# Performance work log

Hardware: AMD Instinct MI355X
Metric: run time of the kernel (lower is better)

## Reference

```python
import jax, jax.numpy as jnp
import numpy as np

# tf.image.rgb_to_grayscale luminance weights
_RGB_W = jnp.array([0.2989, 0.5870, 0.1140], dtype=jnp.float32)
# LBP weight kernel (row-major over the 3x3 neighborhood)
_LBP_K = jnp.array([[1.0, 2.0, 4.0],
                    [128.0, 0.0, 8.0],
                    [64.0, 32.0, 16.0]], dtype=jnp.float32)


def setup_inputs() -> dict:
    key = jax.random.key(0)
    inputs = jax.random.uniform(key, (32, 512, 512, 3), dtype=jnp.float32)
    return {"inputs": inputs}


def reference(inputs):
    # inputs: [N, H, W, 3]
    gray = jnp.tensordot(inputs, _RGB_W, axes=[[-1], [0]])  # [N, H, W]
    N, H, W = gray.shape
    padded = jnp.pad(gray, ((0, 0), (1, 1), (1, 1)))  # SAME zero padding
    # extract_patches(3x3, SAME) -> 9 channels in row-major (dy, dx) order
    patches = jnp.stack(
        [padded[:, dy:dy + H, dx:dx + W] for dy in range(3) for dx in range(3)],
        axis=-1,
    )  # [N, H, W, 9]
    center = patches[..., 4:5]
    binary = jnp.where(patches >= center, 1.0, 0.0)  # [N, H, W, 9]
    # Original conv2d tiles the SAME 3x3 spatial kernel across all 9 input
    # channels, so it equals: (sum over channels) then a 3x3 weighted sum.
    s = binary.sum(axis=-1)  # [N, H, W]
    sp = jnp.pad(s, ((0, 0), (1, 1), (1, 1)))  # SAME zero padding for conv
    lbp = sum(
        _LBP_K[dy, dx] * sp[:, dy:dy + H, dx:dx + W]
        for dy in range(3) for dx in range(3)
        if _LBP_K[dy, dx] != 0.0
    )
    return lbp[..., None]  # [N, H, W, 1]
```

## Files before the change

kernel.cpp:

```cpp
#include <hip/hip_runtime.h>


#define TPB    256
#define TILE_X 64
#define TILE_Y 32
#define GROWS  36
#define GCOLS  72
#define SROWS  34
#define SCOLS  68

typedef float f32x4 __attribute__((ext_vector_type(4)));

__global__ __launch_bounds__(TPB) void lbp_kernel(const float* __restrict__ in,
                                                  float* __restrict__ out) {
    __shared__ float grayS[GROWS * GCOLS];
    __shared__ float sS[SROWS * SCOLS];

    const int n   = blockIdx.z;
    const int y0  = blockIdx.y * TILE_Y;
    const int x0  = blockIdx.x * TILE_X;
    const int tid = threadIdx.x;

    #pragma unroll
    for (int k = 0; k < 3; ++k) {
        const int i = tid + k * TPB;
        if (i < GROWS * (GCOLS / 4)) {
            const int qy  = i / (GCOLS / 4);
            const int qx  = i - qy * (GCOLS / 4);
            const int gy  = y0 - 2 + qy;
            const int px0 = x0 - 4 + qx * 4;
            const bool oky = (unsigned)gy  < 512u;
            const bool okx = (unsigned)px0 < 512u;
            const int  cy  = min(max(gy, 0), 511);
            const int  cx  = okx ? px0 : 0;
            const f32x4* p4 = reinterpret_cast<const f32x4*>(
                in + ((size_t)(n * 512 + cy) * 512 + (size_t)cx) * 3);
            const f32x4 f0 = p4[0];
            const f32x4 f1 = p4[1];
            const f32x4 f2 = p4[2];
            const bool ok = okx & oky;
            const float g0 = __builtin_fmaf(f0.z, 0.114f, __builtin_fmaf(f0.y, 0.587f, f0.x * 0.2989f));
            const float g1 = __builtin_fmaf(f1.y, 0.114f, __builtin_fmaf(f1.x, 0.587f, f0.w * 0.2989f));
            const float g2 = __builtin_fmaf(f2.x, 0.114f, __builtin_fmaf(f1.w, 0.587f, f1.z * 0.2989f));
            const float g3 = __builtin_fmaf(f2.w, 0.114f, __builtin_fmaf(f2.z, 0.587f, f2.y * 0.2989f));
            f32x4 gv;
            gv.x = ok ? g0 : 0.0f;
            gv.y = ok ? g1 : 0.0f;
            gv.z = ok ? g2 : 0.0f;
            gv.w = ok ? g3 : 0.0f;
            *reinterpret_cast<f32x4*>(&grayS[qy * GCOLS + qx * 4]) = gv;
        }
    }
    __syncthreads();

    #pragma unroll
    for (int k = 0; k < 3; ++k) {
        const int i = tid + k * TPB;
        if (i < SROWS * (SCOLS / 4)) {
            const int ly  = i / (SCOLS / 4);
            const int lx0 = (i - ly * (SCOLS / 4)) * 4;
            const f32x4 a0 = *reinterpret_cast<const f32x4*>(&grayS[(ly + 0) * GCOLS + lx0]);
            const f32x4 b0 = *reinterpret_cast<const f32x4*>(&grayS[(ly + 0) * GCOLS + lx0 + 4]);
            const f32x4 a1 = *reinterpret_cast<const f32x4*>(&grayS[(ly + 1) * GCOLS + lx0]);
            const f32x4 b1 = *reinterpret_cast<const f32x4*>(&grayS[(ly + 1) * GCOLS + lx0 + 4]);
            const f32x4 a2 = *reinterpret_cast<const f32x4*>(&grayS[(ly + 2) * GCOLS + lx0]);
            const f32x4 b2 = *reinterpret_cast<const f32x4*>(&grayS[(ly + 2) * GCOLS + lx0 + 4]);
            const float r0[8] = {a0.x, a0.y, a0.z, a0.w, b0.x, b0.y, b0.z, b0.w};
            const float r1[8] = {a1.x, a1.y, a1.z, a1.w, b1.x, b1.y, b1.z, b1.w};
            const float r2[8] = {a2.x, a2.y, a2.z, a2.w, b2.x, b2.y, b2.z, b2.w};
            float sv[4];
            #pragma unroll
            for (int e = 0; e < 4; ++e) {
                const float c = r1[3 + e];
                float s = 0.0f;
                #pragma unroll
                for (int d = 0; d < 3; ++d) {
                    s += (r0[2 + e + d] >= c) ? 1.0f : 0.0f;
                    s += (r1[2 + e + d] >= c) ? 1.0f : 0.0f;
                    s += (r2[2 + e + d] >= c) ? 1.0f : 0.0f;
                }
                const bool ok = ((unsigned)(y0 - 1 + ly) < 512u) &
                                ((unsigned)(x0 - 1 + lx0 + e) < 512u);
                sv[e] = ok ? s : 0.0f;
            }
            f32x4 svv;
            svv.x = sv[0]; svv.y = sv[1]; svv.z = sv[2]; svv.w = sv[3];
            *reinterpret_cast<f32x4*>(&sS[ly * SCOLS + lx0]) = svv;
        }
    }
    __syncthreads();

    #pragma unroll
    for (int k = 0; k < 2; ++k) {
        const int i   = tid + k * TPB;
        const int py  = i / (TILE_X / 4);
        const int px0 = (i - py * (TILE_X / 4)) * 4;
        const f32x4 a0 = *reinterpret_cast<const f32x4*>(&sS[(py + 0) * SCOLS + px0]);
        const f32x4 b0 = *reinterpret_cast<const f32x4*>(&sS[(py + 0) * SCOLS + px0 + 4]);
        const f32x4 a1 = *reinterpret_cast<const f32x4*>(&sS[(py + 1) * SCOLS + px0]);
        const f32x4 b1 = *reinterpret_cast<const f32x4*>(&sS[(py + 1) * SCOLS + px0 + 4]);
        const f32x4 a2 = *reinterpret_cast<const f32x4*>(&sS[(py + 2) * SCOLS + px0]);
        const f32x4 b2 = *reinterpret_cast<const f32x4*>(&sS[(py + 2) * SCOLS + px0 + 4]);
        const float r0[8] = {a0.x, a0.y, a0.z, a0.w, b0.x, b0.y, b0.z, b0.w};
        const float r1[8] = {a1.x, a1.y, a1.z, a1.w, b1.x, b1.y, b1.z, b1.w};
        const float r2[8] = {a2.x, a2.y, a2.z, a2.w, b2.x, b2.y, b2.z, b2.w};
        f32x4 ov;
        #pragma unroll
        for (int e = 0; e < 4; ++e) {
            ov[e] =   1.0f * r0[e] +   2.0f * r0[e + 1] +  4.0f * r0[e + 2]
                  + 128.0f * r1[e] +                        8.0f * r1[e + 2]
                  +  64.0f * r2[e] +  32.0f * r2[e + 1] + 16.0f * r2[e + 2];
        }
        f32x4* dst = reinterpret_cast<f32x4*>(
            out + (size_t)(n * 512 + (y0 + py)) * 512 + (size_t)(x0 + px0));
        __builtin_nontemporal_store(ov, dst);
    }
}

extern "C" void kernel_launch(void* const* d_in, const int* in_sizes, int n_in,
                              void* d_out, int out_size, void* d_ws, size_t ws_size,
                              hipStream_t stream) {
    const float* in = (const float*)d_in[0];
    float* out = (float*)d_out;
    dim3 grid(512 / TILE_X, 512 / TILE_Y, 32);
    dim3 block(TPB);
    lbp_kernel<<<grid, block, 0, stream>>>(in, out);
}
```

Before: 31.33 us.

## Process two images per block and prefetch the second image's input during compute

```diff
diff --git a/kernel.cpp b/kernel.cpp
--- a/kernel.cpp
+++ b/kernel.cpp
@@ -8,113 +8,152 @@
 #define GCOLS  72
 #define SROWS  34
 #define SCOLS  68
+#define GQ     (GROWS * (GCOLS / 4))
+#define SQ     (SROWS * (SCOLS / 4))
 
 typedef float f32x4 __attribute__((ext_vector_type(4)));
 
-__global__ __launch_bounds__(TPB) void lbp_kernel(const float* __restrict__ in,
-                                                  float* __restrict__ out) {
+__global__ __launch_bounds__(TPB, 5) void lbp_kernel(const float* __restrict__ in,
+                                                     float* __restrict__ out) {
     __shared__ float grayS[GROWS * GCOLS];
     __shared__ float sS[SROWS * SCOLS];
 
-    const int n   = blockIdx.z;
     const int y0  = blockIdx.y * TILE_Y;
     const int x0  = blockIdx.x * TILE_X;
     const int tid = threadIdx.x;
+    const int n0  = blockIdx.z;
+    const int n1  = blockIdx.z + 16;
 
-    #pragma unroll
-    for (int k = 0; k < 3; ++k) {
-        const int i = tid + k * TPB;
-        if (i < GROWS * (GCOLS / 4)) {
-            const int qy  = i / (GCOLS / 4);
-            const int qx  = i - qy * (GCOLS / 4);
-            const int gy  = y0 - 2 + qy;
-            const int px0 = x0 - 4 + qx * 4;
-            const bool oky = (unsigned)gy  < 512u;
-            const bool okx = (unsigned)px0 < 512u;
-            const int  cy  = min(max(gy, 0), 511);
-            const int  cx  = okx ? px0 : 0;
-            const f32x4* p4 = reinterpret_cast<const f32x4*>(
-                in + ((size_t)(n * 512 + cy) * 512 + (size_t)cx) * 3);
-            const f32x4 f0 = p4[0];
-            const f32x4 f1 = p4[1];
-            const f32x4 f2 = p4[2];
-            const bool ok = okx & oky;
-            const float g0 = __builtin_fmaf(f0.z, 0.114f, __builtin_fmaf(f0.y, 0.587f, f0.x * 0.2989f));
-            const float g1 = __builtin_fmaf(f1.y, 0.114f, __builtin_fmaf(f1.x, 0.587f, f0.w * 0.2989f));
-            const float g2 = __builtin_fmaf(f2.x, 0.114f, __builtin_fmaf(f1.w, 0.587f, f1.z * 0.2989f));
-            const float g3 = __builtin_fmaf(f2.w, 0.114f, __builtin_fmaf(f2.z, 0.587f, f2.y * 0.2989f));
-            f32x4 gv;
-            gv.x = ok ? g0 : 0.0f;
-            gv.y = ok ? g1 : 0.0f;
-            gv.z = ok ? g2 : 0.0f;
-            gv.w = ok ? g3 : 0.0f;
-            *reinterpret_cast<f32x4*>(&grayS[qy * GCOLS + qx * 4]) = gv;
+    f32x4 L[3][3];
+
+    auto issue = [&](int n) {
+        #pragma unroll
+        for (int k = 0; k < 3; ++k) {
+            const int i = tid + k * TPB;
+            if (i < GQ) {
+                const int qy  = i / (GCOLS / 4);
+                const int qx  = i - qy * (GCOLS / 4);
+                const int gy  = y0 - 2 + qy;
+                const int px0 = x0 - 4 + qx * 4;
+                const bool okx = (unsigned)px0 < 512u;
+                const int  cy  = min(max(gy, 0), 511);
+                const int  cx  = okx ? px0 : 0;
+                const f32x4* p4 = reinterpret_cast<const f32x4*>(
+                    in + ((size_t)(n * 512 + cy) * 512 + (size_t)cx) * 3);
+                L[k][0] = p4[0];
+                L[k][1] = p4[1];
+                L[k][2] = p4[2];
+            }
         }
-    }
-    __syncthreads();
+    };
 
-    #pragma unroll
-    for (int k = 0; k < 3; ++k) {
-        const int i = tid + k * TPB;
-        if (i < SROWS * (SCOLS / 4)) {
-            const int ly  = i / (SCOLS / 4);
-            const int lx0 = (i - ly * (SCOLS / 4)) * 4;
-            const f32x4 a0 = *reinterpret_cast<const f32x4*>(&grayS[(ly + 0) * GCOLS + lx0]);
-            const f32x4 b0 = *reinterpret_cast<const f32x4*>(&grayS[(ly + 0) * GCOLS + lx0 + 4]);
-            const f32x4 a1 = *reinterpret_cast<const f32x4*>(&grayS[(ly + 1) * GCOLS + lx0]);
-            const f32x4 b1 = *reinterpret_cast<const f32x4*>(&grayS[(ly + 1) * GCOLS + lx0 + 4]);
-            const f32x4 a2 = *reinterpret_cast<const f32x4*>(&grayS[(ly + 2) * GCOLS + lx0]);
-            const f32x4 b2 = *reinterpret_cast<const f32x4*>(&grayS[(ly + 2) * GCOLS + lx0 + 4]);
+    auto store_gray = [&]() {
+        #pragma unroll
+        for (int k = 0; k < 3; ++k) {
+            const int i = tid + k * TPB;
+            if (i < GQ) {
+                const int qy  = i / (GCOLS / 4);
+                const int qx  = i - qy * (GCOLS / 4);
+                const int gy  = y0 - 2 + qy;
+                const int px0 = x0 - 4 + qx * 4;
+                const bool ok = ((unsigned)gy < 512u) & ((unsigned)px0 < 512u);
+                const f32x4 f0 = L[k][0], f1 = L[k][1], f2 = L[k][2];
+                const float g0 = __builtin_fmaf(f0.z, 0.114f, __builtin_fmaf(f0.y, 0.587f, f0.x * 0.2989f));
+                const float g1 = __builtin_fmaf(f1.y, 0.114f, __builtin_fmaf(f1.x, 0.587f, f0.w * 0.2989f));
+                const float g2 = __builtin_fmaf(f2.x, 0.114f, __builtin_fmaf(f1.w, 0.587f, f1.z * 0.2989f));
+                const float g3 = __builtin_fmaf(f2.w, 0.114f, __builtin_fmaf(f2.z, 0.587f, f2.y * 0.2989f));
+                f32x4 gv;
+                gv.x = ok ? g0 : 0.0f;
+                gv.y = ok ? g1 : 0.0f;
+                gv.z = ok ? g2 : 0.0f;
+                gv.w = ok ? g3 : 0.0f;
+                *reinterpret_cast<f32x4*>(&grayS[qy * GCOLS + qx * 4]) = gv;
+            }
+        }
+    };
+
+    auto compute_s = [&]() {
+        #pragma unroll
+        for (int k = 0; k < 3; ++k) {
+            const int i = tid + k * TPB;
+            if (i < SQ) {
+                const int ly  = i / (SCOLS / 4);
+                const int lx0 = (i - ly * (SCOLS / 4)) * 4;
+                const f32x4 a0 = *reinterpret_cast<const f32x4*>(&grayS[(ly + 0) * GCOLS + lx0]);
+                const f32x4 b0 = *reinterpret_cast<const f32x4*>(&grayS[(ly + 0) * GCOLS + lx0 + 4]);
+                const f32x4 a1 = *reinterpret_cast<const f32x4*>(&grayS[(ly + 1) * GCOLS + lx0]);
+                const f32x4 b1 = *reinterpret_cast<const f32x4*>(&grayS[(ly + 1) * GCOLS + lx0 + 4]);
+                const f32x4 a2 = *reinterpret_cast<const f32x4*>(&grayS[(ly + 2) * GCOLS + lx0]);
+                const f32x4 b2 = *reinterpret_cast<const f32x4*>(&grayS[(ly + 2) * GCOLS + lx0 + 4]);
+                const float r0[8] = {a0.x, a0.y, a0.z, a0.w, b0.x, b0.y, b0.z, b0.w};
+                const float r1[8] = {a1.x, a1.y, a1.z, a1.w, b1.x, b1.y, b1.z, b1.w};
+                const float r2[8] = {a2.x, a2.y, a2.z, a2.w, b2.x, b2.y, b2.z, b2.w};
+                float sv[4];
+                #pragma unroll
+                for (int e = 0; e < 4; ++e) {
+                    const float c = r1[3 + e];
+                    float s = 0.0f;
+                    #pragma unroll
+                    for (int d = 0; d < 3; ++d) {
+                        s += (r0[2 + e + d] >= c) ? 1.0f : 0.0f;
+                        s += (r1[2 + e + d] >= c) ? 1.0f : 0.0f;
+                        s += (r2[2 + e + d] >= c) ? 1.0f : 0.0f;
+                    }
+                    const bool ok = ((unsigned)(y0 - 1 + ly) < 512u) &
+                                    ((unsigned)(x0 - 1 + lx0 + e) < 512u);
+                    sv[e] = ok ? s : 0.0f;
+                }
+                f32x4 svv;
+                svv.x = sv[0]; svv.y = sv[1]; svv.z = sv[2]; svv.w = sv[3];
+                *reinterpret_cast<f32x4*>(&sS[ly * SCOLS + lx0]) = svv;
+            }
+        }
+    };
+
+    auto lbp_store = [&](int n) {
+        #pragma unroll
+        for (int k = 0; k < 2; ++k) {
+            const int i   = tid + k * TPB;
+            const int py  = i / (TILE_X / 4);
+            const int px0 = (i - py * (TILE_X / 4)) * 4;
+            const f32x4 a0 = *reinterpret_cast<const f32x4*>(&sS[(py + 0) * SCOLS + px0]);
+            const f32x4 b0 = *reinterpret_cast<const f32x4*>(&sS[(py + 0) * SCOLS + px0 + 4]);
+            const f32x4 a1 = *reinterpret_cast<const f32x4*>(&sS[(py + 1) * SCOLS + px0]);
+            const f32x4 b1 = *reinterpret_cast<const f32x4*>(&sS[(py + 1) * SCOLS + px0 + 4]);
+            const f32x4 a2 = *reinterpret_cast<const f32x4*>(&sS[(py + 2) * SCOLS + px0]);
+            const f32x4 b2 = *reinterpret_cast<const f32x4*>(&sS[(py + 2) * SCOLS + px0 + 4]);
             const float r0[8] = {a0.x, a0.y, a0.z, a0.w, b0.x, b0.y, b0.z, b0.w};
             const float r1[8] = {a1.x, a1.y, a1.z, a1.w, b1.x, b1.y, b1.z, b1.w};
             const float r2[8] = {a2.x, a2.y, a2.z, a2.w, b2.x, b2.y, b2.z, b2.w};
-            float sv[4];
+            f32x4 ov;
             #pragma unroll
             for (int e = 0; e < 4; ++e) {
-                const float c = r1[3 + e];
-                float s = 0.0f;
-                #pragma unroll
-                for (int d = 0; d < 3; ++d) {
-                    s += (r0[2 + e + d] >= c) ? 1.0f : 0.0f;
-                    s += (r1[2 + e + d] >= c) ? 1.0f : 0.0f;
-                    s += (r2[2 + e + d] >= c) ? 1.0f : 0.0f;
-                }
-                const bool ok = ((unsigned)(y0 - 1 + ly) < 512u) &
-                                ((unsigned)(x0 - 1 + lx0 + e) < 512u);
-                sv[e] = ok ? s : 0.0f;
+                ov[e] =   1.0f * r0[e] +   2.0f * r0[e + 1] +  4.0f * r0[e + 2]
+                      + 128.0f * r1[e] +                        8.0f * r1[e + 2]
+                      +  64.0f * r2[e] +  32.0f * r2[e + 1] + 16.0f * r2[e + 2];
             }
-            f32x4 svv;
-            svv.x = sv[0]; svv.y = sv[1]; svv.z = sv[2]; svv.w = sv[3];
-            *reinterpret_cast<f32x4*>(&sS[ly * SCOLS + lx0]) = svv;
+            f32x4* dst = reinterpret_cast<f32x4*>(
+                out + (size_t)(n * 512 + (y0 + py)) * 512 + (size_t)(x0 + px0));
+            __builtin_nontemporal_store(ov, dst);
         }
-    }
+    };
+
+    issue(n0);
+    store_gray();
     __syncthreads();
 
-    #pragma unroll
-    for (int k = 0; k < 2; ++k) {
-        const int i   = tid + k * TPB;
-        const int py  = i / (TILE_X / 4);
-        const int px0 = (i - py * (TILE_X / 4)) * 4;
-        const f32x4 a0 = *reinterpret_cast<const f32x4*>(&sS[(py + 0) * SCOLS + px0]);
-        const f32x4 b0 = *reinterpret_cast<const f32x4*>(&sS[(py + 0) * SCOLS + px0 + 4]);
-        const f32x4 a1 = *reinterpret_cast<const f32x4*>(&sS[(py + 1) * SCOLS + px0]);
-        const f32x4 b1 = *reinterpret_cast<const f32x4*>(&sS[(py + 1) * SCOLS + px0 + 4]);
-        const f32x4 a2 = *reinterpret_cast<const f32x4*>(&sS[(py + 2) * SCOLS + px0]);
-        const f32x4 b2 = *reinterpret_cast<const f32x4*>(&sS[(py + 2) * SCOLS + px0 + 4]);
-        const float r0[8] = {a0.x, a0.y, a0.z, a0.w, b0.x, b0.y, b0.z, b0.w};
-        const float r1[8] = {a1.x, a1.y, a1.z, a1.w, b1.x, b1.y, b1.z, b1.w};
-        const float r2[8] = {a2.x, a2.y, a2.z, a2.w, b2.x, b2.y, b2.z, b2.w};
-        f32x4 ov;
-        #pragma unroll
-        for (int e = 0; e < 4; ++e) {
-            ov[e] =   1.0f * r0[e] +   2.0f * r0[e + 1] +  4.0f * r0[e + 2]
-                  + 128.0f * r1[e] +                        8.0f * r1[e + 2]
-                  +  64.0f * r2[e] +  32.0f * r2[e + 1] + 16.0f * r2[e + 2];
-        }
-        f32x4* dst = reinterpret_cast<f32x4*>(
-            out + (size_t)(n * 512 + (y0 + py)) * 512 + (size_t)(x0 + px0));
-        __builtin_nontemporal_store(ov, dst);
-    }
+    issue(n1);
+    compute_s();
+    __syncthreads();
+
+    lbp_store(n0);
+    store_gray();
+    __syncthreads();
+
+    compute_s();
+    __syncthreads();
+
+    lbp_store(n1);
 }
 
 extern "C" void kernel_launch(void* const* d_in, const int* in_sizes, int n_in,
@@ -122,7 +161,7 @@
                               hipStream_t stream) {
     const float* in = (const float*)d_in[0];
     float* out = (float*)d_out;
-    dim3 grid(512 / TILE_X, 512 / TILE_Y, 32);
+    dim3 grid(512 / TILE_X, 512 / TILE_Y, 16);
     dim3 block(TPB);
     lbp_kernel<<<grid, block, 0, stream>>>(in, out);
 }
```

Result: slower. 32.16 us (+2.6%).
